# Kernel tuning notes

Hardware: AMD Instinct MI355X
Metric: run time of the kernel (lower is better)

The kernel has to match this reference:

```python
import jax, jax.numpy as jnp
import numpy as np
import math

D = 512; H = 8; DH = D // H; DFF = 4 * D
B = 128; S = 100; N_LAYERS = 6; VOCAB = 300 + 3
SCALE = 1.0 / math.sqrt(DH)


def _sinusoid(positions, d):
    # standard sinusoidal encoding, valid for negative (relative) positions too
    div = jnp.exp(jnp.arange(0, d, 2, dtype=jnp.float32) * (-math.log(10000.0) / d))
    ang = positions[:, None].astype(jnp.float32) * div[None, :]
    pe = jnp.zeros((positions.shape[0], d), dtype=jnp.float32)
    pe = pe.at[:, 0::2].set(jnp.sin(ang))
    pe = pe.at[:, 1::2].set(jnp.cos(ang))
    return pe


def _layernorm(x, g, b):
    m = jnp.mean(x, -1, keepdims=True)
    v = jnp.mean(jnp.square(x - m), -1, keepdims=True)
    return (x - m) * jax.lax.rsqrt(v + 1e-5) * g + b


def setup_inputs():
    key = jax.random.key(0)
    ks = jax.random.split(key, 16)
    s = 0.05
    n = lambda i, shape: jax.random.normal(ks[i], shape, dtype=jnp.float32) * s
    return {
        'input_ids': jax.random.randint(ks[0], (B, S), 0, VOCAB, dtype=jnp.int32),
        'src_len': jax.random.randint(ks[1], (B,), 1, S + 1, dtype=jnp.int32),
        'emb': n(2, (VOCAB, D)),
        'Wq': n(3, (D, D)), 'Wkv': n(4, (D, 2 * D)), 'Wpos': n(5, (D, D)), 'Wout': n(6, (D, D)),
        'u': n(7, (H, DH)), 'v': n(8, (H, DH)),
        'nmerge_g': jnp.ones((D,), jnp.float32), 'nmerge_b': jnp.zeros((D,), jnp.float32),
        'p1_w': n(9, (D, DFF)), 'p1_b': jnp.zeros((DFF,), jnp.float32),
        'p2_w': n(10, (DFF, D)), 'p2_b': jnp.zeros((D,), jnp.float32),
        'g1_w': n(11, (D, D)), 'g1_b': jnp.zeros((D,), jnp.float32),
        'g2_w': n(12, (D, D)), 'g2_b': jnp.full((D,), -3.0, jnp.float32),
    }


def _rel_attention(x, key_mask, Wq, Wkv, Wout, u, v, k_pos, rel_idx):
    # x: [B,S,D]; key_mask: [B,S] True = padded (masked out)
    q = (x @ Wq).reshape(B, S, H, DH)
    kv = (x @ Wkv).reshape(B, S, H, 2 * DH)
    k, vv = kv[..., :DH], kv[..., DH:]
    content = jnp.einsum('bqhd,bkhd->bhqk', q + u, k)
    pos = jnp.einsum('bqhd,rhd->bhqr', q + v, k_pos)               # r: 2S-1 relative offsets
    pos = jnp.take_along_axis(pos, rel_idx[None, None], axis=-1)   # [B,H,S,S] via rel-shift
    scores = (content + pos) * SCALE
    scores = jnp.where(key_mask[:, None, None, :], -1e9, scores)
    att = jax.nn.softmax(scores, axis=-1)
    out = jnp.einsum('bhqk,bkhd->bqhd', att, vv).reshape(B, S, D)
    return out @ Wout


def reference(input_ids, src_len, emb, Wq, Wkv, Wpos, Wout, u, v, nmerge_g, nmerge_b, p1_w, p1_b, p2_w, p2_b, g1_w, g1_b, g2_w, g2_b):
    # embedding + absolute sinusoidal positional encoding (scale=1.0)
    src = emb[input_ids] + _sinusoid(jnp.arange(S), D)[None]
    key_mask = jnp.arange(S)[None, :] >= src_len[:, None]          # True = masked
    # relative-position keys: offsets q-k ordered S-1 .. -(S-1)
    rel = jnp.arange(S - 1, -S, -1)
    k_pos = (_sinusoid(rel, D) @ Wpos).reshape(2 * S - 1, H, DH)
    i = jnp.arange(S)
    rel_idx = (S - 1) - i[:, None] + i[None, :]                    # (q,k) -> index of offset q-k
    for _ in range(N_LAYERS):  # universal transformer: one shared layer applied N times
        a = _rel_attention(src, key_mask, Wq, Wkv, Wout, u, v, k_pos, rel_idx)
        net = _layernorm(src + a, nmerge_g, nmerge_b)
        proj = jnp.tanh(jax.nn.relu(net @ p1_w + p1_b) @ p2_w + p2_b)
        bgate = jax.nn.sigmoid(jax.nn.relu(net @ g1_w + g1_b) @ g2_w + g2_b)
        src = src * (1.0 - bgate) + proj * bgate                   # NDR gated residual
    return src
```

## Files before the change

### kernel.cpp

```cpp
#include <hip/hip_runtime.h>
#include <hip/hip_bf16.h>
#include <math.h>

#define BB 128
#define SS 100
#define DD 512
#define HH 8
#define DHH 64
#define DFFF 2048
#define RR 199
#define MM (BB*SS)
#define NLAYERS 6
#define SCALE_ 0.125f

typedef __attribute__((ext_vector_type(8))) short bf16x8;
typedef __attribute__((ext_vector_type(4))) float floatx4;

__device__ inline unsigned short f2bf(float f) {
    union { float f; unsigned u; } c; c.f = f;
    unsigned r = c.u + 0x7FFFu + ((c.u >> 16) & 1u);
    return (unsigned short)(r >> 16);
}
__device__ inline float bf2f(unsigned short h) {
    union { unsigned u; float f; } c; c.u = ((unsigned)h) << 16;
    return c.f;
}
__device__ inline void split8(const float* x, bf16x8& hi, bf16x8& lo) {
    #pragma unroll
    for (int i = 0; i < 8; i++) {
        unsigned short h_ = f2bf(x[i]);
        hi[i] = (short)h_;
        lo[i] = (short)f2bf(x[i] - bf2f(h_));
    }
}
__device__ inline void gl2lds16(const unsigned short* g, unsigned short* l) {
    __builtin_amdgcn_global_load_lds(
        (const __attribute__((address_space(1))) void*)g,
        (__attribute__((address_space(3))) void*)l, 16, 0, 0);
}

#define PANEL(buf, rows, r_, k_) ((buf) + ((size_t)((k_) >> 3) * (rows) + (r_)) * 8 + ((k_) & 7))

__global__ void embed_kernel(const int* __restrict__ ids, const float* __restrict__ emb,
                             float* __restrict__ src, unsigned short* __restrict__ srcbf) {
    int r  = blockIdx.x;
    int s  = r % SS;
    int id = ids[r];
    int d0 = threadIdx.x * 4;
    const float c = logf(10000.0f) / 512.0f;
    unsigned short pk[4];
    #pragma unroll
    for (int jj = 0; jj < 4; jj++) {
        int d  = d0 + jj;
        int j2 = d & ~1;
        float freq = expf(-(float)j2 * c);
        float ang  = (float)s * freq;
        float pe   = (d & 1) ? cosf(ang) : sinf(ang);
        float x = emb[id * DD + d] + pe;
        src[r * DD + d] = x;
        pk[jj] = f2bf(x);
    }
    *(uint2*)PANEL(srcbf, MM, r, d0) = *(uint2*)pk;
}

__global__ void kpos_kernel(const float* __restrict__ Wpos, unsigned short* __restrict__ kp) {
    int r = blockIdx.x;
    float p = (float)(SS - 1 - r);
    __shared__ float pe[DD];
    int t = threadIdx.x;
    const float c = logf(10000.0f) / 512.0f;
    {
        int j2 = t & ~1;
        float freq = expf(-(float)j2 * c);
        float ang  = p * freq;
        pe[t] = (t & 1) ? cosf(ang) : sinf(ang);
    }
    __syncthreads();
    float acc = 0.0f;
    for (int k = 0; k < DD; k++) acc += pe[k] * Wpos[k * DD + t];
    kp[r * DD + t] = f2bf(acc);
}

__global__ void wtr_kernel(const float* __restrict__ W, unsigned short* __restrict__ Wt,
                           int K, int N) {
    int idx = blockIdx.x * 256 + threadIdx.x;
    if (idx >= K * N) return;
    int k = idx / N, n = idx - k * N;
    *PANEL(Wt, N, n, k) = f2bf(W[idx]);
}

template<int ACT, int CMODE, int BN>
__global__ __launch_bounds__(256) void mgemm(const unsigned short* __restrict__ A,
                                             const unsigned short* __restrict__ Bt,
                                             const float* __restrict__ bias,
                                             float* __restrict__ Cf,
                                             unsigned short* __restrict__ Cb,
                                             int M, int N, int K) {
    const int NF = BN / 32;
    int nm = M >> 7, nn = N / BN;
    int bid = blockIdx.x;
    int xcd = bid & 7, slot = bid >> 3;
    int c0 = (xcd * nm) >> 3, c1 = ((xcd + 1) * nm) >> 3;
    int cm = c1 - c0;
    if (slot >= cm * nn) return;
    int m0 = (c0 + (slot % cm)) * 128;
    int n0 = (slot / cm) * BN;

    __shared__ __align__(16) unsigned short As[4 * 128 * 8];
    __shared__ __align__(16) unsigned short Bs[4 * BN * 8];
    int t = threadIdx.x, lane = t & 63, wave = t >> 6;
    int quad = lane >> 4, l16 = lane & 15;
    int wm = (wave & 1) * 64, wn = (wave >> 1) * (BN / 2);

    floatx4 acc[4][4];
    #pragma unroll
    for (int i = 0; i < 4; i++)
        #pragma unroll
        for (int j = 0; j < NF; j++) acc[i][j] = (floatx4){0.f, 0.f, 0.f, 0.f};

    for (int k0 = 0; k0 < K; k0 += 32) {
        __syncthreads();
        {
            const unsigned short* gA = A + ((size_t)((k0 >> 3) + wave) * M + m0) * 8;
            unsigned short* lA = As + wave * 128 * 8;
            gl2lds16(gA + lane * 8,        lA + lane * 8);
            gl2lds16(gA + (64 + lane) * 8, lA + (64 + lane) * 8);
        }
        {
            const unsigned short* gB = Bt + ((size_t)((k0 >> 3) + wave) * N + n0) * 8;
            unsigned short* lB = Bs + wave * BN * 8;
            gl2lds16(gB + lane * 8, lB + lane * 8);
            if (BN == 128) gl2lds16(gB + (64 + lane) * 8, lB + (64 + lane) * 8);
        }
        __syncthreads();
        bf16x8 af[4], bfv[4];
        #pragma unroll
        for (int mf = 0; mf < 4; mf++)
            af[mf] = *(const bf16x8*)(As + (quad * 128 + wm + mf * 16 + l16) * 8);
        #pragma unroll
        for (int nf = 0; nf < NF; nf++)
            bfv[nf] = *(const bf16x8*)(Bs + (quad * BN + wn + nf * 16 + l16) * 8);
        #pragma unroll
        for (int mf = 0; mf < 4; mf++)
            #pragma unroll
            for (int nf = 0; nf < NF; nf++)
                acc[mf][nf] = __builtin_amdgcn_mfma_f32_16x16x32_bf16(
                                  af[mf], bfv[nf], acc[mf][nf], 0, 0, 0);
    }

    #pragma unroll
    for (int nf = 0; nf < NF; nf++) {
        int col = n0 + wn + nf * 16 + l16;
        float bv = bias ? bias[col] : 0.0f;
        #pragma unroll
        for (int mf = 0; mf < 4; mf++) {
            #pragma unroll
            for (int r = 0; r < 4; r++) {
                int row = m0 + wm + mf * 16 + quad * 4 + r;
                float x = acc[mf][nf][r] + bv;
                if (ACT == 1) x = fmaxf(x, 0.0f);
                else if (ACT == 2) x = tanhf(x);
                else if (ACT == 3) x = 1.0f / (1.0f + expf(-x));
                if (CMODE == 0)      Cf[(size_t)row * N + col] = x;
                else if (CMODE == 1) *PANEL(Cb, M, row, col) = f2bf(x);
                else                 Cb[(size_t)row * N + col] = f2bf(x);
            }
        }
    }
}
static inline int mgemm_grid(int M, int N, int BN) {
    int nm = M >> 7, nn = N / BN;
    int cmmax = 0;
    for (int x = 0; x < 8; x++) {
        int c = ((x + 1) * nm) / 8 - (x * nm) / 8;
        if (c > cmmax) cmmax = c;
    }
    return 8 * cmmax * nn;
}

#define KPST 72
#define VTST 136
#define PSST 136
__global__ __launch_bounds__(256) void attn_kernel2(
        const float* __restrict__ q, const unsigned short* __restrict__ kvb,
        const unsigned short* __restrict__ kpbf, const float* __restrict__ u,
        const float* __restrict__ v, const int* __restrict__ len_,
        unsigned short* __restrict__ outp) {
    int b = blockIdx.x >> 3, h = blockIdx.x & 7;
    __shared__ __align__(16) unsigned short K_s[112 * KPST];
    __shared__ __align__(16) unsigned short Kp_s[199 * KPST];
    __shared__ __align__(16) unsigned short V_t[64 * VTST];
    __shared__ __align__(16) unsigned short wsc[4][16 * PSST];

    int t = threadIdx.x, wave = t >> 6, lane = t & 63;
    int quad = lane >> 4, l16 = lane & 15;

    for (int idx = t; idx < 112 * 16; idx += 256) {
        int j = idx >> 4, d4 = (idx & 15) * 4;
        uint2 kk = make_uint2(0u, 0u);
        if (j < 100)
            kk = *(const uint2*)(kvb + (((size_t)(b * SS + j)) * HH + h) * 128 + d4);
        *(uint2*)(K_s + j * KPST + d4) = kk;
    }
    for (int idx = t; idx < 199 * 16; idx += 256) {
        int r = idx >> 4, d4 = (idx & 15) * 4;
        *(uint2*)(Kp_s + r * KPST + d4) =
            *(const uint2*)(kpbf + (size_t)r * DD + h * 64 + d4);
    }
    for (int idx = t; idx < 128 * 64; idx += 256) {
        int j = idx >> 6, d = idx & 63;
        unsigned short vv = 0;
        if (j < 100) vv = kvb[(((size_t)(b * SS + j)) * HH + h) * 128 + 64 + d];
        V_t[d * VTST + j] = vv;
    }
    int len = len_[b];
    float ua[2][8], va[2][8];
    #pragma unroll
    for (int kf = 0; kf < 2; kf++)
        #pragma unroll
        for (int i = 0; i < 8; i++) {
            ua[kf][i] = u[h * 64 + kf * 32 + quad * 8 + i];
            va[kf][i] = v[h * 64 + kf * 32 + quad * 8 + i];
        }
    unsigned short* psc = wsc[wave];
    __syncthreads();

    for (int s = wave; s < 7; s += 4) {
        int iq = s * 16 + l16; if (iq > 99) iq = 99;
        const float* qrow = q + ((size_t)(b * SS + iq)) * DD + h * 64;
        bf16x8 qu_h[2], qu_l[2], qv_h[2], qv_l[2];
        #pragma unroll
        for (int kf = 0; kf < 2; kf++) {
            float4 q0 = *(const float4*)(qrow + kf * 32 + quad * 8);
            float4 q1 = *(const float4*)(qrow + kf * 32 + quad * 8 + 4);
            float qa[8] = {q0.x, q0.y, q0.z, q0.w, q1.x, q1.y, q1.z, q1.w};
            float xu[8], xv[8];
            #pragma unroll
            for (int i = 0; i < 8; i++) { xu[i] = qa[i] + ua[kf][i]; xv[i] = qa[i] + va[kf][i]; }
            split8(xu, qu_h[kf], qu_l[kf]);
            split8(xv, qv_h[kf], qv_l[kf]);
        }
        floatx4 cacc[7];
        #pragma unroll
        for (int nt = 0; nt < 7; nt++) cacc[nt] = (floatx4){0.f, 0.f, 0.f, 0.f};
        #pragma unroll
        for (int nt = 0; nt < 7; nt++)
            #pragma unroll
            for (int kf = 0; kf < 2; kf++) {
                bf16x8 kb = *(const bf16x8*)(K_s + (nt * 16 + l16) * KPST + kf * 32 + quad * 8);
                cacc[nt] = __builtin_amdgcn_mfma_f32_16x16x32_bf16(qu_h[kf], kb, cacc[nt], 0, 0, 0);
                cacc[nt] = __builtin_amdgcn_mfma_f32_16x16x32_bf16(qu_l[kf], kb, cacc[nt], 0, 0, 0);
            }
        int w0 = 84 - 16 * s; w0 = w0 < 0 ? 0 : (w0 > 71 ? 71 : w0);
        {
            floatx4 pacc[8];
            #pragma unroll
            for (int nt = 0; nt < 8; nt++) pacc[nt] = (floatx4){0.f, 0.f, 0.f, 0.f};
            #pragma unroll
            for (int nt = 0; nt < 8; nt++)
                #pragma unroll
                for (int kf = 0; kf < 2; kf++) {
                    bf16x8 pb = *(const bf16x8*)(Kp_s + (w0 + nt * 16 + l16) * KPST + kf * 32 + quad * 8);
                    pacc[nt] = __builtin_amdgcn_mfma_f32_16x16x32_bf16(qv_h[kf], pb, pacc[nt], 0, 0, 0);
                    pacc[nt] = __builtin_amdgcn_mfma_f32_16x16x32_bf16(qv_l[kf], pb, pacc[nt], 0, 0, 0);
                }
            #pragma unroll
            for (int nt = 0; nt < 8; nt++)
                #pragma unroll
                for (int r = 0; r < 4; r++)
                    psc[(quad * 4 + r) * PSST + nt * 16 + l16] = f2bf(pacc[nt][r]);
        }
        float sc[7][4];
        #pragma unroll
        for (int nt = 0; nt < 7; nt++)
            #pragma unroll
            for (int r = 0; r < 4; r++) {
                int irow = s * 16 + quad * 4 + r;
                int j = nt * 16 + l16;
                int ro = 99 - irow + j - w0;
                ro = ro < 0 ? 0 : (ro > 135 ? 135 : ro);
                float val = (cacc[nt][r] + bf2f(psc[(quad * 4 + r) * PSST + ro])) * SCALE_;
                sc[nt][r] = (j < len) ? val : -1e9f;
            }
        float inv[4];
        #pragma unroll
        for (int r = 0; r < 4; r++) {
            float m_ = sc[0][r];
            #pragma unroll
            for (int nt = 1; nt < 7; nt++) m_ = fmaxf(m_, sc[nt][r]);
            #pragma unroll
            for (int o = 8; o; o >>= 1) m_ = fmaxf(m_, __shfl_xor(m_, o));
            float s_ = 0.f;
            #pragma unroll
            for (int nt = 0; nt < 7; nt++) { sc[nt][r] = expf(sc[nt][r] - m_); s_ += sc[nt][r]; }
            #pragma unroll
            for (int o = 8; o; o >>= 1) s_ += __shfl_xor(s_, o);
            inv[r] = 1.0f / s_;
        }
        floatx4 oacc[4];
        #pragma unroll
        for (int ntd = 0; ntd < 4; ntd++) oacc[ntd] = (floatx4){0.f, 0.f, 0.f, 0.f};
        #pragma unroll
        for (int pass = 0; pass < 2; pass++) {
            #pragma unroll
            for (int r = 0; r < 4; r++) {
                int row = quad * 4 + r;
                #pragma unroll
                for (int nt = 0; nt < 7; nt++) {
                    float pv = sc[nt][r] * inv[r];
                    unsigned short ph = f2bf(pv);
                    psc[row * PSST + nt * 16 + l16] =
                        (pass == 0) ? ph : f2bf(pv - bf2f(ph));
                }
                psc[row * PSST + 112 + l16] = 0;
            }
            bf16x8 pa[4];
            #pragma unroll
            for (int kf = 0; kf < 4; kf++)
                pa[kf] = *(const bf16x8*)(psc + l16 * PSST + kf * 32 + quad * 8);
            #pragma unroll
            for (int ntd = 0; ntd < 4; ntd++)
                #pragma unroll
                for (int kf = 0; kf < 4; kf++) {
                    bf16x8 bv = *(const bf16x8*)(V_t + (ntd * 16 + l16) * VTST + kf * 32 + quad * 8);
                    oacc[ntd] = __builtin_amdgcn_mfma_f32_16x16x32_bf16(pa[kf], bv, oacc[ntd], 0, 0, 0);
                }
        }
        #pragma unroll
        for (int ntd = 0; ntd < 4; ntd++)
            #pragma unroll
            for (int r = 0; r < 4; r++) {
                int irow = s * 16 + quad * 4 + r;
                if (irow < 100) {
                    int col = h * 64 + ntd * 16 + l16;
                    int row = b * SS + irow;
                    *PANEL(outp, MM, row, col) = f2bf(oacc[ntd][r]);
                }
            }
    }
}

__global__ void ln_kernel(const float* __restrict__ x, const float* __restrict__ a,
                          const float* __restrict__ g, const float* __restrict__ bb,
                          unsigned short* __restrict__ outp) {
    int r = blockIdx.x;
    int t = threadIdx.x;
    float4 xv = *(const float4*)(x + (size_t)r * DD + t * 4);
    float4 av = *(const float4*)(a + (size_t)r * DD + t * 4);
    float v0 = xv.x + av.x, v1 = xv.y + av.y, v2 = xv.z + av.z, v3 = xv.w + av.w;
    float sum = v0 + v1 + v2 + v3;
    float sq  = v0 * v0 + v1 * v1 + v2 * v2 + v3 * v3;
    #pragma unroll
    for (int o = 32; o > 0; o >>= 1) {
        sum += __shfl_down(sum, o);
        sq  += __shfl_down(sq, o);
    }
    __shared__ float ls[2], lq[2];
    if ((t & 63) == 0) { ls[t >> 6] = sum; lq[t >> 6] = sq; }
    __syncthreads();
    float S_ = ls[0] + ls[1], Q_ = lq[0] + lq[1];
    float m   = S_ / 512.0f;
    float var = Q_ / 512.0f - m * m;
    float rs  = rsqrtf(var + 1e-5f);
    float4 gv = *(const float4*)(g  + t * 4);
    float4 bv = *(const float4*)(bb + t * 4);
    unsigned short pk[4];
    pk[0] = f2bf((v0 - m) * rs * gv.x + bv.x);
    pk[1] = f2bf((v1 - m) * rs * gv.y + bv.y);
    pk[2] = f2bf((v2 - m) * rs * gv.z + bv.z);
    pk[3] = f2bf((v3 - m) * rs * gv.w + bv.w);
    *(uint2*)PANEL(outp, MM, r, t * 4) = *(uint2*)pk;
}

__global__ void combine_kernel(float* __restrict__ src, const float* __restrict__ bg,
                               const float* __restrict__ proj,
                               unsigned short* __restrict__ srcbf) {
    int r = blockIdx.x, t = threadIdx.x;
    size_t off = (size_t)r * DD + t * 4;
    float4 s = *(const float4*)(src + off);
    float4 g = *(const float4*)(bg + off);
    float4 p = *(const float4*)(proj + off);
    s.x = s.x * (1.0f - g.x) + p.x * g.x;
    s.y = s.y * (1.0f - g.y) + p.y * g.y;
    s.z = s.z * (1.0f - g.z) + p.z * g.z;
    s.w = s.w * (1.0f - g.w) + p.w * g.w;
    *(float4*)(src + off) = s;
    unsigned short pk[4] = {f2bf(s.x), f2bf(s.y), f2bf(s.z), f2bf(s.w)};
    *(uint2*)PANEL(srcbf, MM, r, t * 4) = *(uint2*)pk;
}

extern "C" void kernel_launch(void* const* d_in, const int* in_sizes, int n_in,
                              void* d_out, int out_size, void* d_ws, size_t ws_size,
                              hipStream_t stream) {
    const int*   ids     = (const int*)  d_in[0];
    const int*   src_len = (const int*)  d_in[1];
    const float* emb     = (const float*)d_in[2];
    const float* Wq      = (const float*)d_in[3];
    const float* Wkv     = (const float*)d_in[4];
    const float* Wpos    = (const float*)d_in[5];
    const float* Wout    = (const float*)d_in[6];
    const float* u       = (const float*)d_in[7];
    const float* v       = (const float*)d_in[8];
    const float* ng      = (const float*)d_in[9];
    const float* nb      = (const float*)d_in[10];
    const float* p1_w    = (const float*)d_in[11];
    const float* p1_b    = (const float*)d_in[12];
    const float* p2_w    = (const float*)d_in[13];
    const float* p2_b    = (const float*)d_in[14];
    const float* g1_w    = (const float*)d_in[15];
    const float* g1_b    = (const float*)d_in[16];
    const float* g2_w    = (const float*)d_in[17];
    const float* g2_b    = (const float*)d_in[18];

    float* src = (float*)d_out;

    float* ws     = (float*)d_ws;
    float* q      = ws;
    float* t1     = q    + (size_t)MM * DD;
    float* proj   = t1   + (size_t)MM * DD;
    float* bg     = proj + (size_t)MM * DD;
    unsigned short* kpbf  = (unsigned short*)(bg + (size_t)MM * DD);
    unsigned short* srcbf = kpbf  + (size_t)RR * DD;
    unsigned short* netbf = srcbf + (size_t)MM * DD;
    unsigned short* t0p   = netbf + (size_t)MM * DD;
    unsigned short* kvb   = t0p   + (size_t)MM * DD;
    unsigned short* ffb   = kvb   + (size_t)MM * 2 * DD;
    unsigned short* hgb   = ffb   + (size_t)MM * DFFF;
    unsigned short* wq_t   = hgb   + (size_t)MM * DD;
    unsigned short* wkv_t  = wq_t   + 512 * 512;
    unsigned short* wout_t = wkv_t  + 1024 * 512;
    unsigned short* p1_t   = wout_t + 512 * 512;
    unsigned short* p2_t   = p1_t   + 2048 * 512;
    unsigned short* g1_t   = p2_t   + 512 * 2048;
    unsigned short* g2_t   = g1_t   + 512 * 512;

    embed_kernel<<<MM, 128, 0, stream>>>(ids, emb, src, srcbf);
    kpos_kernel<<<RR, DD, 0, stream>>>(Wpos, kpbf);
    wtr_kernel<<<(512*512 +255)/256, 256, 0, stream>>>(Wq,   wq_t,   512, 512);
    wtr_kernel<<<(512*1024+255)/256, 256, 0, stream>>>(Wkv,  wkv_t,  512, 1024);
    wtr_kernel<<<(512*512 +255)/256, 256, 0, stream>>>(Wout, wout_t, 512, 512);
    wtr_kernel<<<(512*2048+255)/256, 256, 0, stream>>>(p1_w, p1_t,   512, 2048);
    wtr_kernel<<<(2048*512+255)/256, 256, 0, stream>>>(p2_w, p2_t,   2048, 512);
    wtr_kernel<<<(512*512 +255)/256, 256, 0, stream>>>(g1_w, g1_t,   512, 512);
    wtr_kernel<<<(512*512 +255)/256, 256, 0, stream>>>(g2_w, g2_t,   512, 512);

    int g64  = mgemm_grid(MM, 512, 64);
    int g128k = mgemm_grid(MM, 1024, 128);
    int g128f = mgemm_grid(MM, 2048, 128);

    for (int layer = 0; layer < NLAYERS; layer++) {
        mgemm<0,0,64><<<g64, 256, 0, stream>>>(
            srcbf, wq_t, (const float*)nullptr, q, (unsigned short*)nullptr, MM, 512, 512);
        mgemm<0,2,128><<<g128k, 256, 0, stream>>>(
            srcbf, wkv_t, (const float*)nullptr, (float*)nullptr, kvb, MM, 1024, 512);
        attn_kernel2<<<BB * HH, 256, 0, stream>>>(q, kvb, kpbf, u, v, src_len, t0p);
        mgemm<0,0,64><<<g64, 256, 0, stream>>>(
            t0p, wout_t, (const float*)nullptr, t1, (unsigned short*)nullptr, MM, 512, 512);
        ln_kernel<<<MM, 128, 0, stream>>>(src, t1, ng, nb, netbf);
        mgemm<1,1,128><<<g128f, 256, 0, stream>>>(
            netbf, p1_t, p1_b, (float*)nullptr, ffb, MM, 2048, 512);
        mgemm<2,0,64><<<g64, 256, 0, stream>>>(
            ffb, p2_t, p2_b, proj, (unsigned short*)nullptr, MM, 512, 2048);
        mgemm<1,1,64><<<g64, 256, 0, stream>>>(
            netbf, g1_t, g1_b, (float*)nullptr, hgb, MM, 512, 512);
        mgemm<3,0,64><<<g64, 256, 0, stream>>>(
            hgb, g2_t, g2_b, bg, (unsigned short*)nullptr, MM, 512, 512);
        combine_kernel<<<MM, 128, 0, stream>>>(src, bg, proj, srcbf);
    }
}
```

Baseline: 2.001 ms.

## Fuse gated combine into g2 GEMM epilogue and rework attention kernel

```diff
diff --git a/kernel.cpp b/kernel.cpp
--- a/kernel.cpp
+++ b/kernel.cpp
@@ -14,6 +14,7 @@
 #define SCALE_ 0.125f
 
 typedef __attribute__((ext_vector_type(8))) short bf16x8;
+typedef __attribute__((ext_vector_type(4))) short bf16x4;
 typedef __attribute__((ext_vector_type(4))) float floatx4;
 
 __device__ inline unsigned short f2bf(float f) {
@@ -37,6 +38,11 @@
     __builtin_amdgcn_global_load_lds(
         (const __attribute__((address_space(1))) void*)g,
         (__attribute__((address_space(3))) void*)l, 16, 0, 0);
+}
+__device__ inline bf16x8 ld8_u8align(const unsigned short* p) {
+    bf16x4 a = *(const bf16x4*)p;
+    bf16x4 b = *(const bf16x4*)(p + 4);
+    return __builtin_shufflevector(a, b, 0, 1, 2, 3, 4, 5, 6, 7);
 }
 
 #define PANEL(buf, rows, r_, k_) ((buf) + ((size_t)((k_) >> 3) * (rows) + (r_)) * 8 + ((k_) & 7))
@@ -95,7 +101,8 @@
                                              const float* __restrict__ bias,
                                              float* __restrict__ Cf,
                                              unsigned short* __restrict__ Cb,
-                                             int M, int N, int K) {
+                                             int M, int N, int K,
+                                             const float* __restrict__ Px) {
     const int NF = BN / 32;
     int nm = M >> 7, nn = N / BN;
     int bid = blockIdx.x;
@@ -160,10 +167,16 @@
                 float x = acc[mf][nf][r] + bv;
                 if (ACT == 1) x = fmaxf(x, 0.0f);
                 else if (ACT == 2) x = tanhf(x);
-                else if (ACT == 3) x = 1.0f / (1.0f + expf(-x));
                 if (CMODE == 0)      Cf[(size_t)row * N + col] = x;
                 else if (CMODE == 1) *PANEL(Cb, M, row, col) = f2bf(x);
-                else                 Cb[(size_t)row * N + col] = f2bf(x);
+                else if (CMODE == 2) Cb[(size_t)row * N + col] = f2bf(x);
+                else {
+                    float xg = 1.0f / (1.0f + expf(-x));
+                    size_t o = (size_t)row * N + col;
+                    float out = Cf[o] * (1.0f - xg) + Px[o] * xg;
+                    Cf[o] = out;
+                    *PANEL(Cb, M, row, col) = f2bf(out);
+                }
             }
         }
     }
@@ -178,40 +191,39 @@
     return 8 * cmmax * nn;
 }
 
-#define KPST 72
-#define VTST 136
-#define PSST 136
-__global__ __launch_bounds__(256) void attn_kernel2(
+#define LKP 0
+#define LK  12800
+#define LV  19456
+#define LPS 27648
+#define PSW 116
+__global__ __launch_bounds__(512, 4) void attn_kernel3(
         const float* __restrict__ q, const unsigned short* __restrict__ kvb,
         const unsigned short* __restrict__ kpbf, const float* __restrict__ u,
         const float* __restrict__ v, const int* __restrict__ len_,
         unsigned short* __restrict__ outp) {
+    __shared__ __align__(16) unsigned short lds[40640];
     int b = blockIdx.x >> 3, h = blockIdx.x & 7;
-    __shared__ __align__(16) unsigned short K_s[112 * KPST];
-    __shared__ __align__(16) unsigned short Kp_s[199 * KPST];
-    __shared__ __align__(16) unsigned short V_t[64 * VTST];
-    __shared__ __align__(16) unsigned short wsc[4][16 * PSST];
-
     int t = threadIdx.x, wave = t >> 6, lane = t & 63;
     int quad = lane >> 4, l16 = lane & 15;
 
-    for (int idx = t; idx < 112 * 16; idx += 256) {
-        int j = idx >> 4, d4 = (idx & 15) * 4;
-        uint2 kk = make_uint2(0u, 0u);
-        if (j < 100)
-            kk = *(const uint2*)(kvb + (((size_t)(b * SS + j)) * HH + h) * 128 + d4);
-        *(uint2*)(K_s + j * KPST + d4) = kk;
-    }
-    for (int idx = t; idx < 199 * 16; idx += 256) {
-        int r = idx >> 4, d4 = (idx & 15) * 4;
-        *(uint2*)(Kp_s + r * KPST + d4) =
-            *(const uint2*)(kpbf + (size_t)r * DD + h * 64 + d4);
-    }
-    for (int idx = t; idx < 128 * 64; idx += 256) {
+    {
+        int r8 = lane >> 3;
+        int cc = (lane & 7) ^ r8;
+        for (int i = wave; i < 25; i += 8) {
+            int row = i * 8 + r8;
+            gl2lds16(kpbf + (size_t)row * DD + h * 64 + cc * 8,
+                     lds + LKP + i * 512 + lane * 8);
+        }
+        for (int i = wave; i < 13; i += 8) {
+            int row = i * 8 + r8;
+            gl2lds16(kvb + (size_t)(b * SS + row) * 1024 + h * 128 + cc * 8,
+                     lds + LK + i * 512 + lane * 8);
+        }
+    }
+    for (int idx = t; idx < 8192; idx += 512) {
         int j = idx >> 6, d = idx & 63;
-        unsigned short vv = 0;
-        if (j < 100) vv = kvb[(((size_t)(b * SS + j)) * HH + h) * 128 + 64 + d];
-        V_t[d * VTST + j] = vv;
+        unsigned short vv = kvb[(size_t)(b * SS + j) * 1024 + h * 128 + 64 + d];
+        lds[LV + d * 128 + (((j >> 3) ^ (d & 15)) << 3) + (j & 7)] = vv;
     }
     int len = len_[b];
     float ua[2][8], va[2][8];
@@ -222,122 +234,137 @@
             ua[kf][i] = u[h * 64 + kf * 32 + quad * 8 + i];
             va[kf][i] = v[h * 64 + kf * 32 + quad * 8 + i];
         }
-    unsigned short* psc = wsc[wave];
     __syncthreads();
-
-    for (int s = wave; s < 7; s += 4) {
-        int iq = s * 16 + l16; if (iq > 99) iq = 99;
-        const float* qrow = q + ((size_t)(b * SS + iq)) * DD + h * 64;
-        bf16x8 qu_h[2], qu_l[2], qv_h[2], qv_l[2];
+    if (wave >= 7) return;
+
+    int s = wave;
+    unsigned short* psc = lds + LPS + wave * (16 * PSW);
+
+    int iq = s * 16 + l16; if (iq > 99) iq = 99;
+    const float* qrow = q + ((size_t)(b * SS + iq)) * DD + h * 64;
+    bf16x8 qu_h[2], qu_l[2], qv_h[2], qv_l[2];
+    #pragma unroll
+    for (int kf = 0; kf < 2; kf++) {
+        float4 q0 = *(const float4*)(qrow + kf * 32 + quad * 8);
+        float4 q1 = *(const float4*)(qrow + kf * 32 + quad * 8 + 4);
+        float qa[8] = {q0.x, q0.y, q0.z, q0.w, q1.x, q1.y, q1.z, q1.w};
+        float xu[8], xv[8];
+        #pragma unroll
+        for (int i = 0; i < 8; i++) { xu[i] = qa[i] + ua[kf][i]; xv[i] = qa[i] + va[kf][i]; }
+        split8(xu, qu_h[kf], qu_l[kf]);
+        split8(xv, qv_h[kf], qv_l[kf]);
+    }
+    floatx4 cacc[7];
+    #pragma unroll
+    for (int nt = 0; nt < 7; nt++) cacc[nt] = (floatx4){0.f, 0.f, 0.f, 0.f};
+    #pragma unroll
+    for (int nt = 0; nt < 7; nt++) {
+        int rr = nt * 16 + l16;
         #pragma unroll
         for (int kf = 0; kf < 2; kf++) {
-            float4 q0 = *(const float4*)(qrow + kf * 32 + quad * 8);
-            float4 q1 = *(const float4*)(qrow + kf * 32 + quad * 8 + 4);
-            float qa[8] = {q0.x, q0.y, q0.z, q0.w, q1.x, q1.y, q1.z, q1.w};
-            float xu[8], xv[8];
-            #pragma unroll
-            for (int i = 0; i < 8; i++) { xu[i] = qa[i] + ua[kf][i]; xv[i] = qa[i] + va[kf][i]; }
-            split8(xu, qu_h[kf], qu_l[kf]);
-            split8(xv, qv_h[kf], qv_l[kf]);
-        }
-        floatx4 cacc[7];
-        #pragma unroll
-        for (int nt = 0; nt < 7; nt++) cacc[nt] = (floatx4){0.f, 0.f, 0.f, 0.f};
+            int ch = kf * 4 + quad;
+            bf16x8 kb = *(const bf16x8*)(lds + LK + rr * 64 + ((ch ^ (rr & 7)) << 3));
+            cacc[nt] = __builtin_amdgcn_mfma_f32_16x16x32_bf16(qu_h[kf], kb, cacc[nt], 0, 0, 0);
+            cacc[nt] = __builtin_amdgcn_mfma_f32_16x16x32_bf16(qu_l[kf], kb, cacc[nt], 0, 0, 0);
+        }
+    }
+    int w0 = 84 - 16 * s; if (w0 < 0) w0 = 0;
+    {
+        floatx4 pacc[8];
+        #pragma unroll
+        for (int nt = 0; nt < 8; nt++) pacc[nt] = (floatx4){0.f, 0.f, 0.f, 0.f};
+        #pragma unroll
+        for (int nt = 0; nt < 8; nt++) {
+            int rr = w0 + nt * 16 + l16;
+            #pragma unroll
+            for (int kf = 0; kf < 2; kf++) {
+                int ch = kf * 4 + quad;
+                bf16x8 pb = *(const bf16x8*)(lds + LKP + rr * 64 + ((ch ^ (rr & 7)) << 3));
+                pacc[nt] = __builtin_amdgcn_mfma_f32_16x16x32_bf16(qv_h[kf], pb, pacc[nt], 0, 0, 0);
+                pacc[nt] = __builtin_amdgcn_mfma_f32_16x16x32_bf16(qv_l[kf], pb, pacc[nt], 0, 0, 0);
+            }
+        }
         #pragma unroll
         for (int nt = 0; nt < 7; nt++)
             #pragma unroll
-            for (int kf = 0; kf < 2; kf++) {
-                bf16x8 kb = *(const bf16x8*)(K_s + (nt * 16 + l16) * KPST + kf * 32 + quad * 8);
-                cacc[nt] = __builtin_amdgcn_mfma_f32_16x16x32_bf16(qu_h[kf], kb, cacc[nt], 0, 0, 0);
-                cacc[nt] = __builtin_amdgcn_mfma_f32_16x16x32_bf16(qu_l[kf], kb, cacc[nt], 0, 0, 0);
+            for (int r = 0; r < 4; r++)
+                psc[(quad * 4 + r) * PSW + nt * 16 + l16] = f2bf(pacc[nt][r]);
+        if (l16 < 4)
+            #pragma unroll
+            for (int r = 0; r < 4; r++)
+                psc[(quad * 4 + r) * PSW + 112 + l16] = f2bf(pacc[7][r]);
+    }
+    float sc[7][4];
+    #pragma unroll
+    for (int nt = 0; nt < 7; nt++)
+        #pragma unroll
+        for (int r = 0; r < 4; r++) {
+            int irow = s * 16 + quad * 4 + r;
+            int j = nt * 16 + l16;
+            int ro = 99 - irow + j - w0;
+            ro = ro < 0 ? 0 : (ro > PSW - 1 ? PSW - 1 : ro);
+            float val = (cacc[nt][r] + bf2f(psc[(quad * 4 + r) * PSW + ro])) * SCALE_;
+            sc[nt][r] = (j < len) ? val : -1e9f;
+        }
+    float inv[4];
+    #pragma unroll
+    for (int r = 0; r < 4; r++) {
+        float m_ = sc[0][r];
+        #pragma unroll
+        for (int nt = 1; nt < 7; nt++) m_ = fmaxf(m_, sc[nt][r]);
+        #pragma unroll
+        for (int o = 8; o; o >>= 1) m_ = fmaxf(m_, __shfl_xor(m_, o));
+        float s_ = 0.f;
+        #pragma unroll
+        for (int nt = 0; nt < 7; nt++) { sc[nt][r] = expf(sc[nt][r] - m_); s_ += sc[nt][r]; }
+        #pragma unroll
+        for (int o = 8; o; o >>= 1) s_ += __shfl_xor(s_, o);
+        inv[r] = 1.0f / s_;
+    }
+    bf16x8 zero8 = (bf16x8){0, 0, 0, 0, 0, 0, 0, 0};
+    floatx4 oacc[4];
+    #pragma unroll
+    for (int ntd = 0; ntd < 4; ntd++) oacc[ntd] = (floatx4){0.f, 0.f, 0.f, 0.f};
+    #pragma unroll
+    for (int pass = 0; pass < 2; pass++) {
+        #pragma unroll
+        for (int r = 0; r < 4; r++) {
+            int row = quad * 4 + r;
+            #pragma unroll
+            for (int nt = 0; nt < 7; nt++) {
+                float pv = sc[nt][r] * inv[r];
+                unsigned short ph = f2bf(pv);
+                psc[row * PSW + nt * 16 + l16] =
+                    (pass == 0) ? ph : f2bf(pv - bf2f(ph));
             }
-        int w0 = 84 - 16 * s; w0 = w0 < 0 ? 0 : (w0 > 71 ? 71 : w0);
-        {
-            floatx4 pacc[8];
-            #pragma unroll
-            for (int nt = 0; nt < 8; nt++) pacc[nt] = (floatx4){0.f, 0.f, 0.f, 0.f};
-            #pragma unroll
-            for (int nt = 0; nt < 8; nt++)
-                #pragma unroll
-                for (int kf = 0; kf < 2; kf++) {
-                    bf16x8 pb = *(const bf16x8*)(Kp_s + (w0 + nt * 16 + l16) * KPST + kf * 32 + quad * 8);
-                    pacc[nt] = __builtin_amdgcn_mfma_f32_16x16x32_bf16(qv_h[kf], pb, pacc[nt], 0, 0, 0);
-                    pacc[nt] = __builtin_amdgcn_mfma_f32_16x16x32_bf16(qv_l[kf], pb, pacc[nt], 0, 0, 0);
-                }
-            #pragma unroll
-            for (int nt = 0; nt < 8; nt++)
-                #pragma unroll
-                for (int r = 0; r < 4; r++)
-                    psc[(quad * 4 + r) * PSST + nt * 16 + l16] = f2bf(pacc[nt][r]);
-        }
-        float sc[7][4];
-        #pragma unroll
-        for (int nt = 0; nt < 7; nt++)
-            #pragma unroll
-            for (int r = 0; r < 4; r++) {
-                int irow = s * 16 + quad * 4 + r;
-                int j = nt * 16 + l16;
-                int ro = 99 - irow + j - w0;
-                ro = ro < 0 ? 0 : (ro > 135 ? 135 : ro);
-                float val = (cacc[nt][r] + bf2f(psc[(quad * 4 + r) * PSST + ro])) * SCALE_;
-                sc[nt][r] = (j < len) ? val : -1e9f;
+        }
+        bf16x8 pa[4];
+        #pragma unroll
+        for (int kf = 0; kf < 3; kf++)
+            pa[kf] = ld8_u8align(psc + l16 * PSW + kf * 32 + quad * 8);
+        pa[3] = (quad < 2) ? ld8_u8align(psc + l16 * PSW + 96 + quad * 8) : zero8;
+        #pragma unroll
+        for (int ntd = 0; ntd < 4; ntd++) {
+            int d = ntd * 16 + l16;
+            #pragma unroll
+            for (int kf = 0; kf < 4; kf++) {
+                int ch = kf * 4 + quad;
+                bf16x8 bv = *(const bf16x8*)(lds + LV + d * 128 + ((ch ^ (d & 15)) << 3));
+                oacc[ntd] = __builtin_amdgcn_mfma_f32_16x16x32_bf16(pa[kf], bv, oacc[ntd], 0, 0, 0);
             }
-        float inv[4];
+        }
+    }
+    #pragma unroll
+    for (int ntd = 0; ntd < 4; ntd++)
         #pragma unroll
         for (int r = 0; r < 4; r++) {
-            float m_ = sc[0][r];
-            #pragma unroll
-            for (int nt = 1; nt < 7; nt++) m_ = fmaxf(m_, sc[nt][r]);
-            #pragma unroll
-            for (int o = 8; o; o >>= 1) m_ = fmaxf(m_, __shfl_xor(m_, o));
-            float s_ = 0.f;
-            #pragma unroll
-            for (int nt = 0; nt < 7; nt++) { sc[nt][r] = expf(sc[nt][r] - m_); s_ += sc[nt][r]; }
-            #pragma unroll
-            for (int o = 8; o; o >>= 1) s_ += __shfl_xor(s_, o);
-            inv[r] = 1.0f / s_;
-        }
-        floatx4 oacc[4];
-        #pragma unroll
-        for (int ntd = 0; ntd < 4; ntd++) oacc[ntd] = (floatx4){0.f, 0.f, 0.f, 0.f};
-        #pragma unroll
-        for (int pass = 0; pass < 2; pass++) {
-            #pragma unroll
-            for (int r = 0; r < 4; r++) {
-                int row = quad * 4 + r;
-                #pragma unroll
-                for (int nt = 0; nt < 7; nt++) {
-                    float pv = sc[nt][r] * inv[r];
-                    unsigned short ph = f2bf(pv);
-                    psc[row * PSST + nt * 16 + l16] =
-                        (pass == 0) ? ph : f2bf(pv - bf2f(ph));
-                }
-                psc[row * PSST + 112 + l16] = 0;
+            int irow = s * 16 + quad * 4 + r;
+            if (irow < 100) {
+                int col = h * 64 + ntd * 16 + l16;
+                int row = b * SS + irow;
+                *PANEL(outp, MM, row, col) = f2bf(oacc[ntd][r]);
             }
-            bf16x8 pa[4];
-            #pragma unroll
-            for (int kf = 0; kf < 4; kf++)
-                pa[kf] = *(const bf16x8*)(psc + l16 * PSST + kf * 32 + quad * 8);
-            #pragma unroll
-            for (int ntd = 0; ntd < 4; ntd++)
-                #pragma unroll
-                for (int kf = 0; kf < 4; kf++) {
-                    bf16x8 bv = *(const bf16x8*)(V_t + (ntd * 16 + l16) * VTST + kf * 32 + quad * 8);
-                    oacc[ntd] = __builtin_amdgcn_mfma_f32_16x16x32_bf16(pa[kf], bv, oacc[ntd], 0, 0, 0);
-                }
-        }
-        #pragma unroll
-        for (int ntd = 0; ntd < 4; ntd++)
-            #pragma unroll
-            for (int r = 0; r < 4; r++) {
-                int irow = s * 16 + quad * 4 + r;
-                if (irow < 100) {
-                    int col = h * 64 + ntd * 16 + l16;
-                    int row = b * SS + irow;
-                    *PANEL(outp, MM, row, col) = f2bf(oacc[ntd][r]);
-                }
-            }
-    }
+        }
 }
 
 __global__ void ln_kernel(const float* __restrict__ x, const float* __restrict__ a,
@@ -370,23 +397,6 @@
     pk[2] = f2bf((v2 - m) * rs * gv.z + bv.z);
     pk[3] = f2bf((v3 - m) * rs * gv.w + bv.w);
     *(uint2*)PANEL(outp, MM, r, t * 4) = *(uint2*)pk;
-}
-
-__global__ void combine_kernel(float* __restrict__ src, const float* __restrict__ bg,
-                               const float* __restrict__ proj,
-                               unsigned short* __restrict__ srcbf) {
-    int r = blockIdx.x, t = threadIdx.x;
-    size_t off = (size_t)r * DD + t * 4;
-    float4 s = *(const float4*)(src + off);
-    float4 g = *(const float4*)(bg + off);
-    float4 p = *(const float4*)(proj + off);
-    s.x = s.x * (1.0f - g.x) + p.x * g.x;
-    s.y = s.y * (1.0f - g.y) + p.y * g.y;
-    s.z = s.z * (1.0f - g.z) + p.z * g.z;
-    s.w = s.w * (1.0f - g.w) + p.w * g.w;
-    *(float4*)(src + off) = s;
-    unsigned short pk[4] = {f2bf(s.x), f2bf(s.y), f2bf(s.z), f2bf(s.w)};
-    *(uint2*)PANEL(srcbf, MM, r, t * 4) = *(uint2*)pk;
 }
 
 extern "C" void kernel_launch(void* const* d_in, const int* in_sizes, int n_in,
@@ -444,27 +454,32 @@
     wtr_kernel<<<(512*512 +255)/256, 256, 0, stream>>>(g1_w, g1_t,   512, 512);
     wtr_kernel<<<(512*512 +255)/256, 256, 0, stream>>>(g2_w, g2_t,   512, 512);
 
-    int g64  = mgemm_grid(MM, 512, 64);
+    int g64   = mgemm_grid(MM, 512, 64);
     int g128k = mgemm_grid(MM, 1024, 128);
     int g128f = mgemm_grid(MM, 2048, 128);
 
     for (int layer = 0; layer < NLAYERS; layer++) {
         mgemm<0,0,64><<<g64, 256, 0, stream>>>(
-            srcbf, wq_t, (const float*)nullptr, q, (unsigned short*)nullptr, MM, 512, 512);
+            srcbf, wq_t, (const float*)nullptr, q, (unsigned short*)nullptr,
+            MM, 512, 512, (const float*)nullptr);
         mgemm<0,2,128><<<g128k, 256, 0, stream>>>(
-            srcbf, wkv_t, (const float*)nullptr, (float*)nullptr, kvb, MM, 1024, 512);
-        attn_kernel2<<<BB * HH, 256, 0, stream>>>(q, kvb, kpbf, u, v, src_len, t0p);
+            srcbf, wkv_t, (const float*)nullptr, (float*)nullptr, kvb,
+            MM, 1024, 512, (const float*)nullptr);
+        attn_kernel3<<<BB * HH, 512, 0, stream>>>(q, kvb, kpbf, u, v, src_len, t0p);
         mgemm<0,0,64><<<g64, 256, 0, stream>>>(
-            t0p, wout_t, (const float*)nullptr, t1, (unsigned short*)nullptr, MM, 512, 512);
+            t0p, wout_t, (const float*)nullptr, t1, (unsigned short*)nullptr,
+            MM, 512, 512, (const float*)nullptr);
         ln_kernel<<<MM, 128, 0, stream>>>(src, t1, ng, nb, netbf);
         mgemm<1,1,128><<<g128f, 256, 0, stream>>>(
-            netbf, p1_t, p1_b, (float*)nullptr, ffb, MM, 2048, 512);
+            netbf, p1_t, p1_b, (float*)nullptr, ffb, MM, 2048, 512,
+            (const float*)nullptr);
         mgemm<2,0,64><<<g64, 256, 0, stream>>>(
-            ffb, p2_t, p2_b, proj, (unsigned short*)nullptr, MM, 512, 2048);
+            ffb, p2_t, p2_b, proj, (unsigned short*)nullptr, MM, 512, 2048,
+            (const float*)nullptr);
         mgemm<1,1,64><<<g64, 256, 0, stream>>>(
-            netbf, g1_t, g1_b, (float*)nullptr, hgb, MM, 512, 512);
-        mgemm<3,0,64><<<g64, 256, 0, stream>>>(
-            hgb, g2_t, g2_b, bg, (unsigned short*)nullptr, MM, 512, 512);
-        combine_kernel<<<MM, 128, 0, stream>>>(src, bg, proj, srcbf);
-    }
-}
+            netbf, g1_t, g1_b, (float*)nullptr, hgb, MM, 512, 512,
+            (const float*)nullptr);
+        mgemm<0,3,64><<<g64, 256, 0, stream>>>(
+            hgb, g2_t, g2_b, src, srcbf, MM, 512, 512, proj);
+    }
+}
```

New measurement: 2.021 ms. About the same (+1.0%).
